# Kernel tuning notes

Measured on AMD Instinct MI355X. Metric: run time of the kernel, lower is better.

Reference implementation:

```python
import jax, jax.numpy as jnp
import numpy as np

N = 50000
E = 800000
IN_CH = 128
HID = 64
HEADS = 2
OUT_CH = 5
NEG_SLOPE = 0.2


def glorot(key, shape):
    fan_in, fan_out = shape[0], shape[-1]
    lim = jnp.sqrt(6.0 / (fan_in + fan_out))
    return jax.random.uniform(key, shape, jnp.float32, -lim, lim)


def setup_inputs() -> dict:
    key = jax.random.key(0)
    ks = jax.random.split(key, 20)
    x = jax.random.normal(ks[0], (N, IN_CH), jnp.float32)
    edge_index = jax.random.randint(ks[1], (2, E), 0, N, jnp.int32)
    edge_attr = jax.random.uniform(ks[2], (E, 1), jnp.float32)
    # layer 1: in=128 -> heads=2, out=64 (concat)
    W1l = glorot(ks[3], (IN_CH, HEADS * HID)); b1l = jnp.zeros((HEADS * HID,), jnp.float32)
    W1r = glorot(ks[4], (IN_CH, HEADS * HID)); b1r = jnp.zeros((HEADS * HID,), jnp.float32)
    W1e = glorot(ks[5], (1, HEADS * HID)); b1e = jnp.zeros((HEADS * HID,), jnp.float32)
    att1 = glorot(ks[6], (HEADS, HID))
    bias1 = jnp.zeros((HEADS * HID,), jnp.float32)
    # layer 2: in=128 -> heads=1, out=5
    W2l = glorot(ks[7], (HEADS * HID, OUT_CH)); b2l = jnp.zeros((OUT_CH,), jnp.float32)
    W2r = glorot(ks[8], (HEADS * HID, OUT_CH)); b2r = jnp.zeros((OUT_CH,), jnp.float32)
    W2e = glorot(ks[9], (1, OUT_CH)); b2e = jnp.zeros((OUT_CH,), jnp.float32)
    att2 = glorot(ks[10], (1, OUT_CH))
    bias2 = jnp.zeros((OUT_CH,), jnp.float32)
    return dict(x=x, edge_index=edge_index, edge_attr=edge_attr,
                W1l=W1l, b1l=b1l, W1r=W1r, b1r=b1r, W1e=W1e, b1e=b1e, att1=att1, bias1=bias1,
                W2l=W2l, b2l=b2l, W2r=W2r, b2r=b2r, W2e=W2e, b2e=b2e, att2=att2, bias2=bias2)


def gatv2_layer(x, src, dst, edge_attr, Wl, bl, Wr, br, We, be, att, bias, heads, out_ch, concat):
    n = x.shape[0]
    xl = (x @ Wl + bl).reshape(n, heads, out_ch)   # source transform
    xr = (x @ Wr + br).reshape(n, heads, out_ch)   # target transform
    ee = (edge_attr @ We + be).reshape(-1, heads, out_ch)
    # GATv2 score: a^T LeakyReLU(xl[src] + xr[dst] + e)
    s = xl[src] + xr[dst] + ee                      # [E, H, C]
    s = jnp.where(s > 0, s, NEG_SLOPE * s)
    logits = jnp.einsum('ehc,hc->eh', s, att)       # [E, H]
    # segment softmax over incoming edges of each destination node
    mx = jax.ops.segment_max(logits, dst, num_segments=n)
    ex = jnp.exp(logits - mx[dst])
    den = jax.ops.segment_sum(ex, dst, num_segments=n)
    alpha = ex / den[dst]                           # [E, H]
    msg = alpha[:, :, None] * xl[src]               # [E, H, C]
    out = jax.ops.segment_sum(msg, dst, num_segments=n)  # [N, H, C]
    if concat:
        out = out.reshape(n, heads * out_ch)
    else:
        out = out.mean(axis=1)
    return out + bias


def reference(x, edge_index, edge_attr,
              W1l, b1l, W1r, b1r, W1e, b1e, att1, bias1,
              W2l, b2l, W2r, b2r, W2e, b2e, att2, bias2):
    src, dst = edge_index[0], edge_index[1]
    h = gatv2_layer(x, src, dst, edge_attr, W1l, b1l, W1r, b1r, W1e, b1e, att1, bias1,
                    HEADS, HID, True)
    h = jax.nn.elu(h)
    out = gatv2_layer(h, src, dst, edge_attr, W2l, b2l, W2r, b2r, W2e, b2e, att2, bias2,
                      1, OUT_CH, True)
    return out
```

## Files before the change

### kernel.cpp

```cpp
#include <hip/hip_runtime.h>
#include <hip/hip_bf16.h>
#include <math.h>

#define NN 50000
#define NE 800000
#define NB 196
#define CAP 64
#define NEG_SLOPE 0.2f
#define LOG2E 1.44269504088896340736f
#define NSB 3125
#define NGB 3125

typedef __attribute__((ext_vector_type(8))) short bf16x8;
typedef __attribute__((ext_vector_type(4))) float f32x4;
typedef __attribute__((ext_vector_type(2))) float f32x2;


__device__ __forceinline__ float ldf(const void* p, long i, int isbf) {
    if (isbf) {
        unsigned short raw = ((const unsigned short*)p)[i];
        return __uint_as_float(((unsigned)raw) << 16);
    }
    return ((const float*)p)[i];
}

__device__ __forceinline__ float2 ldf2(const void* p, long i2, int isbf) {
    if (isbf) {
        unsigned raw = ((const unsigned*)p)[i2];
        return make_float2(__uint_as_float(raw << 16),
                           __uint_as_float(raw & 0xffff0000u));
    }
    return ((const float2*)p)[i2];
}

__device__ __forceinline__ short f2bs(float f) {
    __hip_bfloat16 h = __float2bfloat16(f);
    short s; __builtin_memcpy(&s, &h, 2); return s;
}
__device__ __forceinline__ unsigned short f2bu(float f) {
    __hip_bfloat16 h = __float2bfloat16(f);
    unsigned short s; __builtin_memcpy(&s, &h, 2); return s;
}

__device__ __forceinline__ float red16(float p) {
    p += __int_as_float(__builtin_amdgcn_update_dpp(
             0, __float_as_int(p), 0xB1, 0xF, 0xF, false));
    p += __int_as_float(__builtin_amdgcn_update_dpp(
             0, __float_as_int(p), 0x4E, 0xF, 0xF, false));
    p += __int_as_float(__builtin_amdgcn_update_dpp(
             0, __float_as_int(p), 0x141, 0xF, 0xF, false));
    p += __int_as_float(__builtin_amdgcn_update_dpp(
             0, __float_as_int(p), 0x140, 0xF, 0xF, false));
    return p;
}

__device__ __forceinline__ float red32(float p) {
    p = red16(p);
    p += __int_as_float(__builtin_amdgcn_ds_swizzle(__float_as_int(p), 0x401F));
    return p;
}

__global__ void k_setup_wprep(const void* x, int* flag, unsigned* cnt,
                              const void* __restrict__ Wl,
                              const void* __restrict__ Wr,
                              unsigned short* __restrict__ bfrag) {
    if (blockIdx.x < NB) {
        int i = blockIdx.x * 256 + threadIdx.x;
        if (i < NN) cnt[i] = 0u;
        return;
    }
    unsigned short raw0 = ((const unsigned short*)x)[(threadIdx.x & 63) * 2];
    float v0 = __uint_as_float(((unsigned)raw0) << 16);
    bool sane = isfinite(v0) && fabsf(v0) > 1e-5f && fabsf(v0) < 1e3f;
    const int isbf = (__popcll(__ballot(sane)) > 32) ? 1 : 0;
    if (blockIdx.x == NB && threadIdx.x == 0) *flag = isbf;
    int idx = (blockIdx.x - NB) * 256 + threadIdx.x;
    int j = idx & 7, lane = (idx >> 3) & 63, ks = (idx >> 9) & 3, nt = idx >> 11;
    int k = ks * 32 + (lane >> 4) * 8 + j;
    int n = nt * 16 + (lane & 15);
    float v = (n < 128) ? ldf(Wl, (long)k * 128 + n, isbf)
                        : ldf(Wr, (long)k * 128 + (n - 128), isbf);
    bfrag[idx] = f2bu(v);
}

__global__ __launch_bounds__(256) void k_lin1_scatter(
    const void* __restrict__ x, const unsigned short* __restrict__ bfrag,
    const void* __restrict__ bl, const void* __restrict__ br,
    const void* __restrict__ be1,
    unsigned short* __restrict__ xl, unsigned short* __restrict__ xr,
    const int* __restrict__ ei, const void* __restrict__ ea,
    unsigned* __restrict__ cnt, unsigned* __restrict__ sedge,
    const int* __restrict__ flag) {
    const int isbf = flag[0];
    if (blockIdx.x < NSB) {
        const int e = blockIdx.x * 256 + threadIdx.x;
        if (e < NE) {
            const int d = ei[NE + e];
            const unsigned pos = atomicAdd(&cnt[d], 1u);
            if (pos < CAP) {
                const float av = ldf(ea, e, isbf);
                sedge[(long)d * CAP + pos] =
                    (__float_as_uint(av) & 0xffff0000u) | (unsigned)ei[e];
            }
        }
        return;
    }
    const int wave = threadIdx.x >> 6, lane = threadIdx.x & 63;
    const int mrow = lane & 15, quad = lane >> 4;
    const long mbase = (long)(blockIdx.x - NSB) * 16;
    bf16x8 afrag[4];
    if (isbf) {
        const unsigned short* xp = (const unsigned short*)x
                                 + (mbase + mrow) * 128 + quad * 8;
#pragma unroll
        for (int ks = 0; ks < 4; ks++)
            afrag[ks] = *(const bf16x8*)(xp + ks * 32);
    } else {
        const float* xp = (const float*)x + (mbase + mrow) * 128 + quad * 8;
#pragma unroll
        for (int ks = 0; ks < 4; ks++) {
            const float4 u0 = *(const float4*)(xp + ks * 32);
            const float4 u1 = *(const float4*)(xp + ks * 32 + 4);
            bf16x8 a;
            a[0] = f2bs(u0.x); a[1] = f2bs(u0.y); a[2] = f2bs(u0.z); a[3] = f2bs(u0.w);
            a[4] = f2bs(u1.x); a[5] = f2bs(u1.y); a[6] = f2bs(u1.z); a[7] = f2bs(u1.w);
            afrag[ks] = a;
        }
    }
#pragma unroll
    for (int q = 0; q < 4; q++) {
        const int nt = wave * 4 + q;
        f32x4 acc = {0.f, 0.f, 0.f, 0.f};
#pragma unroll
        for (int ks = 0; ks < 4; ks++) {
            const bf16x8 bfr = *(const bf16x8*)(bfrag + ((nt * 4 + ks) * 64 + lane) * 8);
            acc = __builtin_amdgcn_mfma_f32_16x16x32_bf16(afrag[ks], bfr, acc, 0, 0, 0);
        }
        const int ng = nt * 16 + (lane & 15);
        const float bv = (ng < 128)
            ? ldf(bl, ng, isbf)
            : ldf(br, ng - 128, isbf) + ldf(be1, ng - 128, isbf);
        unsigned short* dst = (ng < 128) ? xl : xr;
        const int col = ng & 127;
#pragma unroll
        for (int reg = 0; reg < 4; reg++) {
            const long row = mbase + quad * 4 + reg;
            dst[row * 128 + col] = f2bu(acc[reg] + bv);
        }
    }
}

__global__ __launch_bounds__(256) void k_attn1(
    const unsigned* __restrict__ deg, const unsigned* __restrict__ sedge,
    const unsigned* __restrict__ xl, const unsigned* __restrict__ xr,
    const void* __restrict__ We, const void* __restrict__ att,
    const void* __restrict__ bias,
    const void* __restrict__ W2l, const void* __restrict__ b2l,
    const void* __restrict__ W2r, const void* __restrict__ b2r,
    const void* __restrict__ b2e,
    unsigned short* __restrict__ xl2b, float* __restrict__ xr2,
    const int* __restrict__ flag) {
    const int isbf = flag[0];
    const int n = blockIdx.x * 4 + (threadIdx.x >> 6);
    if (n >= NN) return;
    const int lane = threadIdx.x & 63;
    const unsigned rraw = xr[(long)n * 64 + lane];
    const f32x2 xrv = {__uint_as_float(rraw << 16),
                       __uint_as_float(rraw & 0xffff0000u)};
    const float2 wet = ldf2(We, lane, isbf);
    const f32x2 wev = {wet.x, wet.y};
    const float2 att_ = ldf2(att, lane, isbf);
    const f32x2 atv = {att_.x * LOG2E, att_.y * LOG2E};
    const f32x2 nsv = {NEG_SLOPE, NEG_SLOPE};
    float lsum[4] = {0.f, 0.f, 0.f, 0.f};
    f32x2 accv[4] = {{0.f, 0.f}, {0.f, 0.f}, {0.f, 0.f}, {0.f, 0.f}};
    const int dg = min((int)deg[n], CAP);
    const long base = (long)n * CAP;
    for (int i = 0; i < dg; i += 4) {
#pragma unroll
        for (int k = 0; k < 4; k++) {
            const int idx = i + k;
            const float valid = (idx < dg) ? 1.f : 0.f;
            const int idxc = (idx < dg) ? idx : dg - 1;
            const unsigned eg = sedge[base + idxc];
            const int s = eg & 0xffffu;
            const float e = __uint_as_float(eg & 0xffff0000u);
            const unsigned rw = xl[(long)s * 64 + lane];
            f32x2 xv;
            xv.x = __uint_as_float(rw << 16);
            xv.y = __uint_as_float(rw & 0xffff0000u);
            f32x2 t = xv + __builtin_elementwise_fma((f32x2){e, e}, wev, xrv);
            t = __builtin_elementwise_max(t, t * nsv);
            const f32x2 pd = t * atv;
            float p = red32(pd.x + pd.y);
            p = fminf(fmaxf(p, -60.f), 60.f);
            const float w = exp2f(p) * valid;
            lsum[k] += w;
            accv[k] = __builtin_elementwise_fma((f32x2){w, w}, xv, accv[k]);
        }
    }
    const float l = (lsum[0] + lsum[1]) + (lsum[2] + lsum[3]);
    const f32x2 av = (accv[0] + accv[1]) + (accv[2] + accv[3]);
    const float inv = 1.f / fmaxf(l, 1e-20f);
    const float2 bsv = ldf2(bias, lane, isbf);
    float h0 = fmaf(av.x, inv, bsv.x);
    float h1 = fmaf(av.y, inv, bsv.y);
    h0 = h0 > 0.f ? h0 : expm1f(h0);
    h1 = h1 > 0.f ? h1 : expm1f(h1);
    float pl[5], pr[5];
#pragma unroll
    for (int c = 0; c < 5; c++) {
        pl[c] = h0 * ldf(W2l, (2 * lane) * 5 + c, isbf)
              + h1 * ldf(W2l, (2 * lane + 1) * 5 + c, isbf);
        pr[c] = h0 * ldf(W2r, (2 * lane) * 5 + c, isbf)
              + h1 * ldf(W2r, (2 * lane + 1) * 5 + c, isbf);
        pl[c] = red16(pl[c]);
        pr[c] = red16(pr[c]);
    }
#pragma unroll
    for (int off = 16; off <= 32; off <<= 1) {
#pragma unroll
        for (int c = 0; c < 5; c++) {
            pl[c] += __shfl_xor(pl[c], off);
            pr[c] += __shfl_xor(pr[c], off);
        }
    }
    if (lane == 0) {
        uint4 pk;
        pk.x = (unsigned)f2bu(pl[0] + ldf(b2l, 0, isbf))
             | ((unsigned)f2bu(pl[1] + ldf(b2l, 1, isbf)) << 16);
        pk.y = (unsigned)f2bu(pl[2] + ldf(b2l, 2, isbf))
             | ((unsigned)f2bu(pl[3] + ldf(b2l, 3, isbf)) << 16);
        pk.z = (unsigned)f2bu(pl[4] + ldf(b2l, 4, isbf));
        pk.w = 0u;
        *(uint4*)(xl2b + (long)n * 8) = pk;
#pragma unroll
        for (int c = 0; c < 5; c++)
            xr2[(long)n * 8 + c] = pr[c] + ldf(b2r, c, isbf) + ldf(b2e, c, isbf);
    }
}

__global__ __launch_bounds__(256) void k_attn2(
    const unsigned* __restrict__ deg, const unsigned* __restrict__ sedge,
    const unsigned short* __restrict__ xl2b, const float* __restrict__ xr2,
    const void* __restrict__ We, const void* __restrict__ att,
    const void* __restrict__ bias,
    void* __restrict__ out, const int* __restrict__ flag) {
    const int isbf = flag[0];
    const int n = blockIdx.x * 16 + (threadIdx.x >> 4);
    if (n >= NN) return;
    const int l16 = threadIdx.x & 15;
    f32x4 xrb4; float xrb4s;
    f32x4 wev4; float wev4s;
    f32x4 atv4; float atv4s;
    {
        const float4 r0 = *(const float4*)(xr2 + (long)n * 8);
        xrb4 = (f32x4){r0.x, r0.y, r0.z, r0.w};
        xrb4s = xr2[(long)n * 8 + 4];
        wev4 = (f32x4){ldf(We, 0, isbf), ldf(We, 1, isbf),
                       ldf(We, 2, isbf), ldf(We, 3, isbf)};
        wev4s = ldf(We, 4, isbf);
        atv4 = (f32x4){ldf(att, 0, isbf), ldf(att, 1, isbf),
                       ldf(att, 2, isbf), ldf(att, 3, isbf)} * (f32x4)LOG2E;
        atv4s = ldf(att, 4, isbf) * LOG2E;
    }
    const f32x4 ns4 = {NEG_SLOPE, NEG_SLOPE, NEG_SLOPE, NEG_SLOPE};
    float lw = 0.f, laccs = 0.f;
    f32x4 lacc4 = {0.f, 0.f, 0.f, 0.f};
    const int dg = min((int)deg[n], CAP);
    const long base = (long)n * CAP;
    for (int idx = l16; idx < dg; idx += 16) {
        const unsigned eg = sedge[base + idx];
        const int s = eg & 0xffffu;
        const float a = __uint_as_float(eg & 0xffff0000u);
        const uint4 u = *(const uint4*)(xl2b + (long)s * 8);
        f32x4 xls4;
        xls4.x = __uint_as_float(u.x << 16);
        xls4.y = __uint_as_float(u.x & 0xffff0000u);
        xls4.z = __uint_as_float(u.y << 16);
        xls4.w = __uint_as_float(u.y & 0xffff0000u);
        const float xlss = __uint_as_float(u.z << 16);
        f32x4 v4 = xls4 + __builtin_elementwise_fma((f32x4){a, a, a, a}, wev4, xrb4);
        v4 = __builtin_elementwise_max(v4, v4 * ns4);
        float vs = xlss + fmaf(a, wev4s, xrb4s);
        vs = fmaxf(vs, NEG_SLOPE * vs);
        const f32x4 pd = v4 * atv4;
        float p = ((pd.x + pd.y) + (pd.z + pd.w)) + vs * atv4s;
        p = fminf(fmaxf(p, -60.f), 60.f);
        const float w = exp2f(p);
        lw += w;
        lacc4 = __builtin_elementwise_fma((f32x4){w, w, w, w}, xls4, lacc4);
        laccs = fmaf(w, xlss, laccs);
    }
    lw = red16(lw);
    lacc4.x = red16(lacc4.x);
    lacc4.y = red16(lacc4.y);
    lacc4.z = red16(lacc4.z);
    lacc4.w = red16(lacc4.w);
    laccs = red16(laccs);
    if (l16 == 0) {
        const float inv = 1.f / fmaxf(lw, 1e-20f);
        float o[5] = {lacc4.x, lacc4.y, lacc4.z, lacc4.w, laccs};
#pragma unroll
        for (int c = 0; c < 5; c++) {
            const float v = fmaf(o[c], inv, ldf(bias, c, isbf));
            if (isbf) ((__hip_bfloat16*)out)[(long)n * 5 + c] = __float2bfloat16(v);
            else      ((float*)out)[(long)n * 5 + c] = v;
        }
    }
}

extern "C" void kernel_launch(void* const* d_in, const int* in_sizes, int n_in,
                              void* d_out, int out_size, void* d_ws, size_t ws_size,
                              hipStream_t stream) {
    const void* x    = d_in[0];
    const int*  ei   = (const int*)d_in[1];
    const void* ea   = d_in[2];
    const void* W1l  = d_in[3];
    const void* b1l  = d_in[4];
    const void* W1r  = d_in[5];
    const void* b1r  = d_in[6];
    const void* W1e  = d_in[7];
    const void* b1e  = d_in[8];
    const void* att1 = d_in[9];
    const void* bias1= d_in[10];
    const void* W2l  = d_in[11];
    const void* b2l  = d_in[12];
    const void* W2r  = d_in[13];
    const void* b2r  = d_in[14];
    const void* W2e  = d_in[15];
    const void* b2e  = d_in[16];
    const void* att2 = d_in[17];
    const void* bias2= d_in[18];

    float* W = (float*)d_ws;
    int*            flag    = (int*)W;
    unsigned*       cnt     = (unsigned*)(W + 60000);
    unsigned*       sedge   = (unsigned*)(W + 120000);
    unsigned short* xl1b    = (unsigned short*)(W + 3400000);
    unsigned short* xr1b    = (unsigned short*)(W + 6600000);
    unsigned short* bfrag   = (unsigned short*)(W + 9800000);
    unsigned short* xl2b    = (unsigned short*)(W + 9900000);
    float*          xr2     = W + 10300000;

    k_setup_wprep<<<NB + 128, 256, 0, stream>>>(x, flag, cnt, W1l, W1r, bfrag);
    k_lin1_scatter<<<NSB + NGB, 256, 0, stream>>>(
        x, bfrag, b1l, b1r, b1e, xl1b, xr1b, ei, ea, cnt, sedge, flag);
    k_attn1<<<(NN + 3) / 4, 256, 0, stream>>>(cnt, sedge,
                                              (const unsigned*)xl1b, (const unsigned*)xr1b,
                                              W1e, att1, bias1,
                                              W2l, b2l, W2r, b2r, b2e, xl2b, xr2, flag);
    k_attn2<<<(NN * 16 + 255) / 256, 256, 0, stream>>>(cnt, sedge, xl2b, xr2,
                                                       W2e, att2, bias2, d_out, flag);
}
```

Baseline: 258.0 us.

## Process four edges per wave with 16-lane groups and 16-byte feature loads

After: 328.6 us. 27.4% more time.

```diff
diff --git a/kernel.cpp b/kernel.cpp
--- a/kernel.cpp
+++ b/kernel.cpp
@@ -54,10 +54,18 @@
     return p;
 }
 
-__device__ __forceinline__ float red32(float p) {
-    p = red16(p);
-    p += __int_as_float(__builtin_amdgcn_ds_swizzle(__float_as_int(p), 0x401F));
+__device__ __forceinline__ float red8(float p) {
+    p += __int_as_float(__builtin_amdgcn_update_dpp(
+             0, __float_as_int(p), 0xB1, 0xF, 0xF, false));
+    p += __int_as_float(__builtin_amdgcn_update_dpp(
+             0, __float_as_int(p), 0x4E, 0xF, 0xF, false));
+    p += __int_as_float(__builtin_amdgcn_update_dpp(
+             0, __float_as_int(p), 0x141, 0xF, 0xF, false));
     return p;
+}
+
+__device__ __forceinline__ float bperm(int addr4, float v) {
+    return __int_as_float(__builtin_amdgcn_ds_bpermute(addr4, __float_as_int(v)));
 }
 
 __global__ void k_setup_wprep(const void* x, int* flag, unsigned* cnt,
@@ -161,50 +169,77 @@
     unsigned short* __restrict__ xl2b, float* __restrict__ xr2,
     const int* __restrict__ flag) {
     const int isbf = flag[0];
-    const int n = blockIdx.x * 4 + (threadIdx.x >> 6);
+    const int n = __builtin_amdgcn_readfirstlane(
+        blockIdx.x * 4 + (threadIdx.x >> 6));
     if (n >= NN) return;
     const int lane = threadIdx.x & 63;
-    const unsigned rraw = xr[(long)n * 64 + lane];
-    const f32x2 xrv = {__uint_as_float(rraw << 16),
-                       __uint_as_float(rraw & 0xffff0000u)};
-    const float2 wet = ldf2(We, lane, isbf);
-    const f32x2 wev = {wet.x, wet.y};
-    const float2 att_ = ldf2(att, lane, isbf);
-    const f32x2 atv = {att_.x * LOG2E, att_.y * LOG2E};
-    const f32x2 nsv = {NEG_SLOPE, NEG_SLOPE};
-    float lsum[4] = {0.f, 0.f, 0.f, 0.f};
-    f32x2 accv[4] = {{0.f, 0.f}, {0.f, 0.f}, {0.f, 0.f}, {0.f, 0.f}};
-    const int dg = min((int)deg[n], CAP);
-    const long base = (long)n * CAP;
-    for (int i = 0; i < dg; i += 4) {
+    const int sub = lane & 15;
+    const int grp = lane >> 4;
+    float xr8[8], we8[8], at8[8];
+    {
+        const uint4 xru = *(const uint4*)(xr + (long)n * 64 + sub * 4);
+        const unsigned uu[4] = {xru.x, xru.y, xru.z, xru.w};
 #pragma unroll
         for (int k = 0; k < 4; k++) {
-            const int idx = i + k;
-            const float valid = (idx < dg) ? 1.f : 0.f;
-            const int idxc = (idx < dg) ? idx : dg - 1;
-            const unsigned eg = sedge[base + idxc];
-            const int s = eg & 0xffffu;
-            const float e = __uint_as_float(eg & 0xffff0000u);
-            const unsigned rw = xl[(long)s * 64 + lane];
-            f32x2 xv;
-            xv.x = __uint_as_float(rw << 16);
-            xv.y = __uint_as_float(rw & 0xffff0000u);
-            f32x2 t = xv + __builtin_elementwise_fma((f32x2){e, e}, wev, xrv);
-            t = __builtin_elementwise_max(t, t * nsv);
-            const f32x2 pd = t * atv;
-            float p = red32(pd.x + pd.y);
-            p = fminf(fmaxf(p, -60.f), 60.f);
-            const float w = exp2f(p) * valid;
-            lsum[k] += w;
-            accv[k] = __builtin_elementwise_fma((f32x2){w, w}, xv, accv[k]);
-        }
-    }
-    const float l = (lsum[0] + lsum[1]) + (lsum[2] + lsum[3]);
-    const f32x2 av = (accv[0] + accv[1]) + (accv[2] + accv[3]);
-    const float inv = 1.f / fmaxf(l, 1e-20f);
+            xr8[2 * k]     = __uint_as_float(uu[k] << 16);
+            xr8[2 * k + 1] = __uint_as_float(uu[k] & 0xffff0000u);
+        }
+#pragma unroll
+        for (int j = 0; j < 8; j++) {
+            we8[j] = ldf(We, sub * 8 + j, isbf);
+            at8[j] = ldf(att, sub * 8 + j, isbf) * LOG2E;
+        }
+    }
+    float lsum = 0.f;
+    float acc[8] = {0.f, 0.f, 0.f, 0.f, 0.f, 0.f, 0.f, 0.f};
+    const int dg = min((int)__builtin_amdgcn_readfirstlane(deg[n]), CAP);
+    const unsigned* __restrict__ sb = sedge + (long)n * CAP;
+    const unsigned vsub = (unsigned)(sub * 16);
+    for (int i = grp; i < dg; i += 4) {
+        const unsigned eg = sb[i];
+        const int s = (int)(eg & 0xffffu);
+        const float e = __uint_as_float(eg & 0xffff0000u);
+        const uint4 u = *(const uint4*)((const char*)xl
+                                        + (((unsigned)s << 8) + vsub));
+        float xv[8];
+        xv[0] = __uint_as_float(u.x << 16); xv[1] = __uint_as_float(u.x & 0xffff0000u);
+        xv[2] = __uint_as_float(u.y << 16); xv[3] = __uint_as_float(u.y & 0xffff0000u);
+        xv[4] = __uint_as_float(u.z << 16); xv[5] = __uint_as_float(u.z & 0xffff0000u);
+        xv[6] = __uint_as_float(u.w << 16); xv[7] = __uint_as_float(u.w & 0xffff0000u);
+        float p = 0.f;
+#pragma unroll
+        for (int j = 0; j < 8; j++) {
+            float t = fmaf(e, we8[j], xv[j] + xr8[j]);
+            t = fmaxf(t, t * NEG_SLOPE);
+            p = fmaf(t, at8[j], p);
+        }
+        p = red8(p);
+        p = fminf(fmaxf(p, -60.f), 60.f);
+        const float w = exp2f(p);
+        lsum += w;
+#pragma unroll
+        for (int j = 0; j < 8; j++) acc[j] = fmaf(w, xv[j], acc[j]);
+    }
+    lsum += __int_as_float(__builtin_amdgcn_ds_swizzle(__float_as_int(lsum), 0x401F));
+    lsum += __shfl_xor(lsum, 32);
+#pragma unroll
+    for (int j = 0; j < 8; j++) {
+        acc[j] += __int_as_float(__builtin_amdgcn_ds_swizzle(__float_as_int(acc[j]), 0x401F));
+        acc[j] += __shfl_xor(acc[j], 32);
+    }
+    const int a4 = (lane >> 2) * 4;
+    const float e0 = bperm(a4, acc[0]), e2 = bperm(a4, acc[2]);
+    const float e4 = bperm(a4, acc[4]), e6 = bperm(a4, acc[6]);
+    const float o1 = bperm(a4, acc[1]), o3 = bperm(a4, acc[3]);
+    const float o5 = bperm(a4, acc[5]), o7 = bperm(a4, acc[7]);
+    const float lsr = bperm(a4, lsum);
+    const int pp = lane & 3;
+    const float av0 = pp < 2 ? (pp == 0 ? e0 : e2) : (pp == 2 ? e4 : e6);
+    const float av1 = pp < 2 ? (pp == 0 ? o1 : o3) : (pp == 2 ? o5 : o7);
+    const float inv = 1.f / fmaxf(lsr, 1e-20f);
     const float2 bsv = ldf2(bias, lane, isbf);
-    float h0 = fmaf(av.x, inv, bsv.x);
-    float h1 = fmaf(av.y, inv, bsv.y);
+    float h0 = fmaf(av0, inv, bsv.x);
+    float h1 = fmaf(av1, inv, bsv.y);
     h0 = h0 > 0.f ? h0 : expm1f(h0);
     h1 = h1 > 0.f ? h1 : expm1f(h1);
     float pl[5], pr[5];
```
